# Optimization experiments

Hardware: AMD Instinct MI355X
Metric: run time of the kernel (lower is better)

The kernel has to match this reference:

```python
import jax, jax.numpy as jnp
import numpy as np
import math

B, S, E, H, FF = 8, 1024, 1024, 16, 4096
HD = E // H
N_DOM = 1024          # boolean-domain size used in the custom scale
LN_EPS = 1e-5


def _layernorm(x, g, b, eps=LN_EPS):
    mu = jnp.mean(x, axis=-1, keepdims=True)
    var = jnp.var(x, axis=-1, keepdims=True)
    return (x - mu) * jax.lax.rsqrt(var + eps) * g + b


def setup_inputs() -> dict:
    key = jax.random.key(0)
    ks = jax.random.split(key, 8)
    s_e = 1.0 / math.sqrt(E)
    s_f = 1.0 / math.sqrt(FF)
    return {
        "x": jax.random.normal(ks[0], (B, S, E), jnp.float32),
        "in_proj_w": jax.random.normal(ks[1], (3 * E, E), jnp.float32) * s_e,
        "out_proj_w": jax.random.normal(ks[2], (E, E), jnp.float32) * s_e,
        "ln1_g": jnp.ones((E,), jnp.float32),
        "ln1_b": jnp.zeros((E,), jnp.float32),
        "ln2_g": jnp.ones((E,), jnp.float32),
        "ln2_b": jnp.zeros((E,), jnp.float32),
        "w1": jax.random.normal(ks[3], (FF, E), jnp.float32) * s_e,
        "b1": jax.random.normal(ks[4], (FF,), jnp.float32) * 0.01,
        "w2": jax.random.normal(ks[5], (E, FF), jnp.float32) * s_f,
        "b2": jax.random.normal(ks[6], (E,), jnp.float32) * 0.01,
    }


def reference(x, in_proj_w, out_proj_w, ln1_g, ln1_b, ln2_g, ln2_b, w1, b1, w2, b2):
    # --- custom multi-head attention (bias=False, dropout=0) ---
    qkv = jnp.einsum("bse,fe->bsf", x, in_proj_w)              # [B,S,3E]
    q, k, v = jnp.split(qkv, 3, axis=-1)
    q = q.reshape(B, S, H, HD)
    k = k.reshape(B, S, H, HD)
    v = v.reshape(B, S, H, HD)
    # nonstandard scale: sqrt(1/head_dim) * 2 * log(N)
    scale = math.sqrt(1.0 / HD) * 2.0 * math.log(N_DOM)
    scores = jnp.einsum("bqhd,bkhd->bhqk", q * scale, k)       # [B,H,S,S]
    attn = jax.nn.softmax(scores, axis=-1)
    ctx = jnp.einsum("bhqk,bkhd->bqhd", attn, v).reshape(B, S, E)
    attn_out = jnp.einsum("bse,fe->bsf", ctx, out_proj_w)      # [B,S,E]
    # --- residual + norm + FFN + residual + norm ---
    h = _layernorm(x + attn_out, ln1_g, ln1_b)
    ff = jnp.einsum("bsf,ef->bse", jax.nn.relu(jnp.einsum("bse,fe->bsf", h, w1) + b1), w2) + b2
    return _layernorm(h + ff, ln2_g, ln2_b)
```

## Files before the change

kernel.cpp:

```cpp
#include <hip/hip_runtime.h>
#include <cstdint>
#include <cmath>


typedef _Float16 f16;
typedef _Float16 f16x8 __attribute__((ext_vector_type(8)));
typedef _Float16 f16x4 __attribute__((ext_vector_type(4)));
typedef __bf16   bf16;
typedef __bf16   bf16x8 __attribute__((ext_vector_type(8)));
typedef __bf16   bf16x4 __attribute__((ext_vector_type(4)));
typedef __bf16   bf16x2 __attribute__((ext_vector_type(2)));
typedef float    f32x4  __attribute__((ext_vector_type(4)));
typedef float    f32x16 __attribute__((ext_vector_type(16)));
typedef unsigned int uint2v __attribute__((ext_vector_type(2)));
typedef unsigned int u32x4v __attribute__((ext_vector_type(4)));

#define B_SZ  8
#define S_SZ  1024
#define E_SZ  1024
#define H_SZ  16
#define HD_SZ 64
#define FF_SZ 4096
#define MTOK  (B_SZ * S_SZ)

__device__ __forceinline__ void async_ld16(const void* g, void* l) {
  __builtin_amdgcn_global_load_lds(
      (const __attribute__((address_space(1))) void*)(uintptr_t)g,
      (__attribute__((address_space(3))) void*)(uint32_t)(uintptr_t)l,
      16, 0, 0);
}

template <int N>
__device__ __forceinline__ void wait_vm() {
  if constexpr (N == 0)      asm volatile("s_waitcnt vmcnt(0)" ::: "memory");
  else if constexpr (N == 3) asm volatile("s_waitcnt vmcnt(3)" ::: "memory");
  else if constexpr (N == 4) asm volatile("s_waitcnt vmcnt(4)" ::: "memory");
  else static_assert(N == 0 || N == 3 || N == 4, "unsupported vmcnt");
  __builtin_amdgcn_sched_barrier(0);
}

__device__ __forceinline__ void wait_lgkm0_fenced() {
  asm volatile("s_waitcnt lgkmcnt(0)" ::: "memory");
  __builtin_amdgcn_sched_barrier(0);
}

__device__ __forceinline__ void permswap(uint32_t& a, uint32_t& b) {
  uint2v r = __builtin_amdgcn_permlane32_swap(a, b, false, false);
  a = r[0];
  b = r[1];
}

__global__ void cast_all_kernel(const float* __restrict__ wqkv, const float* __restrict__ wo,
                                const float* __restrict__ w1, const float* __restrict__ w2,
                                const float* __restrict__ x,
                                f16* __restrict__ w_inb, f16* __restrict__ w_outb,
                                f16* __restrict__ w1b, f16* __restrict__ w2b,
                                f16* __restrict__ xb) {
  const int i = blockIdx.x * blockDim.x + threadIdx.x;
  const float* src;
  f16* dst;
  int off;
  if (i < 786432)       { src = wqkv; dst = w_inb;  off = i; }
  else if (i < 1048576) { src = wo;   dst = w_outb; off = i - 786432; }
  else if (i < 2097152) { src = w1;   dst = w1b;    off = i - 1048576; }
  else if (i < 3145728) { src = w2;   dst = w2b;    off = i - 2097152; }
  else                  { src = x;    dst = xb;     off = i - 3145728; }
  float4 f = ((const float4*)src)[off];
  f16x4 o = {(f16)f.x, (f16)f.y, (f16)f.z, (f16)f.w};
  ((f16x4*)dst)[off] = o;
}

template <int BN, bool OUT_F16, bool RELU>
__global__ __launch_bounds__(512, 2)
void gemm256(const f16* __restrict__ A, const f16* __restrict__ Bm,
             const float* __restrict__ bias, void* __restrict__ Cp,
             int M, int N, int K, int bf16_from_col) {
  static_assert(BN == 256 || BN == 128, "BN must be 256 or 128");
  static_assert(!(OUT_F16 && BN == 128), "f16 LDS epilogue requires BN==256");
  constexpr int NBCH  = (BN == 256) ? 2 : 1;
  constexpr int CHUNK = 4096;
  constexpr int NIF   = 2 + NBCH;
  constexpr int WN    = (BN == 256) ? 4 : 2;
  constexpr int FM    = (BN == 256) ? 8 : 4;

  __shared__ f16 lds[(8 + 4 * NBCH) * CHUNK];
  f16* Ab = lds;
  f16* Bb = lds + 8 * CHUNK;

  const int tid  = threadIdx.x;
  const int wave = tid >> 6;
  const int lane = tid & 63;
  const int quad = lane >> 4;
  const int l16  = lane & 15;

  const int wm  = wave / WN;
  const int wn  = wave % WN;
  const int ah  = (BN == 256) ? wm : (wm >> 1);
  const int amB = (BN == 256) ? 0 : (wm & 1) * 64;
  const int bh  = (BN == 256) ? (wn >> 1) : 0;
  const int bnB = (BN == 256) ? (wn & 1) * 64 : wn * 64;

  const int gx = N / BN;
  int bm, bn;
  {
    const int b   = blockIdx.x;
    const int nwg = gridDim.x;
    const int gm  = nwg / gx;
    if (((nwg & 63) == 0) && ((gx & 1) == 0) && ((gm & 3) == 0)) {
      const int xcd = b & 7;
      const int seq = b >> 3;
      const int st  = xcd + ((seq >> 3) << 3);
      const int pos = seq & 7;
      const int nstx = gx >> 1;
      bn = (st % nstx) * 2 + (pos & 1);
      bm = (st / nstx) * 4 + (pos >> 1);
    } else {
      int logical = b;
      if ((nwg & 7) == 0) logical = (logical & 7) * (nwg >> 3) + (logical >> 3);
      bn = logical % gx;
      bm = logical / gx;
    }
  }

  f32x4 acc[FM][4];
#pragma unroll
  for (int mi = 0; mi < FM; mi++)
#pragma unroll
    for (int ni = 0; ni < 4; ni++) acc[mi][ni] = (f32x4){0.f, 0.f, 0.f, 0.f};

  const int rr_s = tid >> 2;
  const int lo_s = (tid & 3) ^ ((rr_s >> 1) & 3);
  const int wofs = wave * 512;
  const f16* gAb = A  + ((size_t)bm * 256 + rr_s) * (size_t)K + lo_s * 8;
  const f16* gBb = Bm + ((size_t)bn * BN  + rr_s) * (size_t)K + lo_s * 8;

  auto stA = [&](int bb, int s, int h, int kt) {
    async_ld16(gAb + (size_t)h * 128 * K + kt * 64 + s * 32,
               Ab + ((((bb << 1) + s) << 1) + h) * CHUNK + wofs);
  };
  auto stB = [&](int bb, int s, int h, int kt) {
    async_ld16(gBb + (size_t)h * 128 * K + kt * 64 + s * 32,
               Bb + (((bb << 1) + s) * NBCH + h) * CHUNK + wofs);
  };
  auto rdFrag = [&](const f16* ch, int rr) -> f16x8 {
    return *(const f16x8*)&ch[rr * 32 + ((quad ^ ((rr >> 1) & 3)) << 3)];
  };

  const int NT = K >> 6;

#pragma unroll
  for (int s = 0; s < 2; s++) {
    stA(0, s, 0, 0);
    stA(0, s, 1, 0);
    stB(0, s, 0, 0);
    if constexpr (NBCH == 2) stB(0, s, 1, 0);
  }
  wait_vm<NIF>();
  __builtin_amdgcn_s_barrier();

  for (int t = 0; t < NT; t++) {
    const int cur = t & 1, oth = cur ^ 1;
    const bool last = (t == NT - 1);
#pragma unroll
    for (int s = 0; s < 2; s++) {
      const f16* Ach = Ab + ((((cur << 1) + s) << 1) + ah) * CHUNK;
      const f16* Bch = Bb + (((cur << 1) + s) * NBCH + bh) * CHUNK;

      f16x8 bfr[4], af[4];
#pragma unroll
      for (int ni = 0; ni < 4; ni++) bfr[ni] = rdFrag(Bch, bnB + ni * 16 + l16);
#pragma unroll
      for (int i = 0; i < 4; i++) af[i] = rdFrag(Ach, amB + i * 16 + l16);
      if (!last) {
        stA(oth, s, 0, t + 1);
        stA(oth, s, 1, t + 1);
        if constexpr (NBCH == 1) stB(oth, s, 0, t + 1);
      }
      __builtin_amdgcn_sched_barrier(0);
      __builtin_amdgcn_s_barrier();
      wait_lgkm0_fenced();
      __builtin_amdgcn_s_setprio(1);
#pragma unroll
      for (int i = 0; i < 4; i++)
#pragma unroll
        for (int ni = 0; ni < 4; ni++)
          acc[i][ni] = __builtin_amdgcn_mfma_f32_16x16x32_f16(bfr[ni], af[i], acc[i][ni], 0, 0, 0);
      __builtin_amdgcn_s_setprio(0);

      if constexpr (BN == 256) {
        __builtin_amdgcn_s_barrier();
#pragma unroll
        for (int i = 0; i < 4; i++) af[i] = rdFrag(Ach, amB + (4 + i) * 16 + l16);
        if (!last) {
          stB(oth, s, 0, t + 1);
          stB(oth, s, 1, t + 1);
        }
        __builtin_amdgcn_sched_barrier(0);
        __builtin_amdgcn_s_barrier();
        wait_lgkm0_fenced();
        __builtin_amdgcn_s_setprio(1);
#pragma unroll
        for (int i = 0; i < 4; i++)
#pragma unroll
          for (int ni = 0; ni < 4; ni++)
            acc[4 + i][ni] = __builtin_amdgcn_mfma_f32_16x16x32_f16(bfr[ni], af[i], acc[4 + i][ni], 0, 0, 0);
        __builtin_amdgcn_s_setprio(0);
      }

      if (!last) {
        wait_vm<NIF>();
        __builtin_amdgcn_s_barrier();
      } else if (s == 0) {
        wait_vm<0>();
        __builtin_amdgcn_s_barrier();
      }
    }
  }

  if constexpr (!OUT_F16) {
    const int rowG0 = bm * 256 + ((BN == 256) ? wm * 128 : wm * 64);
    const int colG0 = bn * BN + wn * 64;
    float* Cf = (float*)Cp;
#pragma unroll
    for (int ni = 0; ni < 4; ni++) {
      const int col = colG0 + ni * 16 + quad * 4;
      float4 bv = {0.f, 0.f, 0.f, 0.f};
      if (bias != nullptr) bv = *(const float4*)&bias[col];
#pragma unroll
      for (int mi = 0; mi < FM; mi++) {
        const int row = rowG0 + mi * 16 + l16;
        float v0 = acc[mi][ni][0] + bv.x;
        float v1 = acc[mi][ni][1] + bv.y;
        float v2 = acc[mi][ni][2] + bv.z;
        float v3 = acc[mi][ni][3] + bv.w;
        if (RELU) {
          v0 = fmaxf(v0, 0.f); v1 = fmaxf(v1, 0.f);
          v2 = fmaxf(v2, 0.f); v3 = fmaxf(v3, 0.f);
        }
        f32x4 o = {v0, v1, v2, v3};
        *(f32x4*)&Cf[(size_t)row * N + col] = o;
      }
    }
  } else {
    __syncthreads();
    {
      char* cb = (char*)lds;
      const int rowL0 = wm * 128;
      const int colL0 = wn * 64;
      const bool store_bf16 = (bn * BN >= bf16_from_col);
#pragma unroll
      for (int mi = 0; mi < FM; mi++) {
        const int row = rowL0 + mi * 16 + l16;
        const int sw  = row & 7;
#pragma unroll
        for (int ni = 0; ni < 4; ni++) {
          const int col = colL0 + ni * 16 + quad * 4;
          float4 bv = {0.f, 0.f, 0.f, 0.f};
          if (bias != nullptr) bv = *(const float4*)&bias[bn * BN + col];
          float v0 = acc[mi][ni][0] + bv.x;
          float v1 = acc[mi][ni][1] + bv.y;
          float v2 = acc[mi][ni][2] + bv.z;
          float v3 = acc[mi][ni][3] + bv.w;
          if (RELU) {
            v0 = fmaxf(v0, 0.f); v1 = fmaxf(v1, 0.f);
            v2 = fmaxf(v2, 0.f); v3 = fmaxf(v3, 0.f);
          }
          const int ch = (col >> 3) ^ sw;
          char* p = cb + row * 512 + (ch << 4) + ((quad & 1) << 3);
          if (store_bf16) {
            bf16x4 o = {(bf16)v0, (bf16)v1, (bf16)v2, (bf16)v3};
            *(bf16x4*)p = o;
          } else {
            f16x4 o = {(f16)v0, (f16)v1, (f16)v2, (f16)v3};
            *(f16x4*)p = o;
          }
        }
      }
    }
    __syncthreads();
    {
      const char* cb = (const char*)lds;
      const int rr0 = tid >> 5;
      const int cc  = tid & 31;
      const size_t rowBytes = (size_t)N * 2;
      char* gbase = (char*)Cp + (size_t)(bm * 256) * rowBytes
                  + (size_t)bn * BN * 2 + (size_t)cc * 16;
#pragma unroll
      for (int it = 0; it < 16; it++) {
        const int row = it * 16 + rr0;
        const int ch  = cc ^ (row & 7);
        u32x4v v = *(const u32x4v*)(cb + row * 512 + (ch << 4));
        *(u32x4v*)(gbase + (size_t)row * rowBytes) = v;
      }
    }
  }
  (void)M;
}

__global__ __launch_bounds__(256, 4)
void attn_kernel(const f16* __restrict__ qkv, f16* __restrict__ ctx,
                 float scale2, float c2) {
  __shared__ __align__(16) char pool[33280];
  f16*  Ks = (f16*)pool;
  bf16* Vt = (bf16*)(pool + 16384);

  const int tid  = threadIdx.x;
  const int wave = tid >> 6;
  const int lane = tid & 63;
  const int l31  = lane & 31;
  const int hi   = lane >> 5;

  const int flat = blockIdx.x;
  const int bh   = flat & 127;
  const int qt   = flat >> 7;
  const int b    = bh >> 4;
  const int h    = bh & 15;

  const int rs = 3 * E_SZ;
  const size_t tokbase = (size_t)b * S_SZ;

  const int su  = lane >> 3;
  const int soc = (lane & 7) ^ su;

  {
    const f16* gq = qkv + (tokbase + qt * 128 + wave * 8 + su) * (size_t)rs + h * HD_SZ + soc * 8;
#pragma unroll
    for (int i = 0; i < 4; i++)
      async_ld16(gq + (size_t)i * 32 * rs, pool + (i * 32 + wave * 8) * 128);
  }
  __syncthreads();

  f16x8 aq[4];
  {
    const int qrow = wave * 32 + l31;
    const f16 sc = (f16)scale2;
    const f16x8 sc8 = {sc, sc, sc, sc, sc, sc, sc, sc};
#pragma unroll
    for (int ks = 0; ks < 4; ks++) {
      f16x8 q = *(const f16x8*)&Ks[qrow * 64 + (((ks * 2 + hi) ^ (qrow & 7)) << 3)];
      aq[ks] = q * sc8;
    }
  }

  f16x8  kreg[4];
  bf16x8 vr0, vr1, vr2, vr3;
  const int vc  = (tid & 7) * 8;
  const int vk0 = (tid >> 3) * 4;
  {
    const f16* gk = qkv + (tokbase + wave * 8 + su) * (size_t)rs + E_SZ + h * HD_SZ + soc * 8;
#pragma unroll
    for (int i = 0; i < 4; i++) kreg[i] = *(const f16x8*)(gk + (size_t)i * 32 * rs);
    const bf16* gv = (const bf16*)qkv + (tokbase + vk0) * (size_t)rs + 2 * E_SZ + h * HD_SZ + vc;
    vr0 = *(const bf16x8*)(gv);
    vr1 = *(const bf16x8*)(gv + rs);
    vr2 = *(const bf16x8*)(gv + 2 * rs);
    vr3 = *(const bf16x8*)(gv + 3 * rs);
  }

  float Lp = 0.f;
  f32x16 oacc[2];
#pragma unroll
  for (int nb = 0; nb < 2; nb++)
#pragma unroll
    for (int i = 0; i < 16; i++) oacc[nb][i] = 0.f;

  const float negc2 = -c2;

  for (int t = 0; t < S_SZ / 128; t++) {
    __syncthreads();
    {
      const int kwr = (wave * 8 + su) * 64 + (lane & 7) * 8;
#pragma unroll
      for (int i = 0; i < 4; i++)
        *(f16x8*)&Ks[kwr + i * 32 * 64] = kreg[i];
    }
    {
#pragma unroll
      for (int e = 0; e < 8; e++) {
        bf16x4 pk = {vr0[e], vr1[e], vr2[e], vr3[e]};
        *(bf16x4*)&Vt[(vc + e) * 132 + vk0] = pk;
      }
    }
    __syncthreads();

    if (t < S_SZ / 128 - 1) {
      const f16* gk = qkv + (tokbase + (t + 1) * 128 + wave * 8 + su) * (size_t)rs + E_SZ + h * HD_SZ + soc * 8;
#pragma unroll
      for (int i = 0; i < 4; i++) kreg[i] = *(const f16x8*)(gk + (size_t)i * 32 * rs);
      const bf16* gv = (const bf16*)qkv + (tokbase + (t + 1) * 128 + vk0) * (size_t)rs + 2 * E_SZ + h * HD_SZ + vc;
      vr0 = *(const bf16x8*)(gv);
      vr1 = *(const bf16x8*)(gv + rs);
      vr2 = *(const bf16x8*)(gv + 2 * rs);
      vr3 = *(const bf16x8*)(gv + 3 * rs);
    }

#pragma unroll
    for (int nt = 0; nt < 4; nt++) {
      f32x16 sacc;
#pragma unroll
      for (int i = 0; i < 16; i++) sacc[i] = negc2;

      const int krow = nt * 32 + l31;
      __builtin_amdgcn_s_setprio(1);
#pragma unroll
      for (int ks = 0; ks < 4; ks++) {
        f16x8 kf = *(const f16x8*)&Ks[krow * 64 + (((ks * 2 + hi) ^ (krow & 7)) << 3)];
        sacc = __builtin_amdgcn_mfma_f32_32x32x16_f16(kf, aq[ks], sacc, 0, 0, 0);
      }
      __builtin_amdgcn_s_setprio(0);

      uint32_t w[8];
#pragma unroll
      for (int j = 0; j < 8; j++) {
        float p0 = exp2f(sacc[2 * j]);
        float p1 = exp2f(sacc[2 * j + 1]);
        Lp += p0 + p1;
        bf16x2 pk2 = {(bf16)p0, (bf16)p1};
        w[j] = __builtin_bit_cast(uint32_t, pk2);
      }
      permswap(w[0], w[2]);
      permswap(w[1], w[3]);
      permswap(w[4], w[6]);
      permswap(w[5], w[7]);
      u32x4v pe = {w[0], w[1], w[2], w[3]};
      u32x4v po = {w[4], w[5], w[6], w[7]};
      bf16x8 pa[2] = {__builtin_bit_cast(bf16x8, pe), __builtin_bit_cast(bf16x8, po)};

      __builtin_amdgcn_s_setprio(1);
#pragma unroll
      for (int nb = 0; nb < 2; nb++) {
        const int d = nb * 32 + l31;
#pragma unroll
        for (int kst = 0; kst < 2; kst++) {
          const int key = (nt * 2 + kst) * 16 + hi * 8;
          bf16x4 blo = *(const bf16x4*)&Vt[d * 132 + key];
          bf16x4 bhi = *(const bf16x4*)&Vt[d * 132 + key + 4];
          bf16x8 bv = __builtin_shufflevector(blo, bhi, 0, 1, 2, 3, 4, 5, 6, 7);
          oacc[nb] = __builtin_amdgcn_mfma_f32_32x32x16_bf16(pa[kst], bv, oacc[nb], 0, 0, 0);
        }
      }
      __builtin_amdgcn_s_setprio(0);
    }
  }

  float Lfull = Lp + __shfl_xor(Lp, 32, 64);
  const float inv = 1.f / Lfull;
#pragma unroll
  for (int r = 0; r < 16; r++) {
    const int qrow = (r & 3) + 8 * (r >> 2) + 4 * hi;
    const float invr = __shfl(inv, qrow, 32);
    const size_t row = tokbase + (size_t)qt * 128 + wave * 32 + qrow;
#pragma unroll
    for (int nb = 0; nb < 2; nb++)
      ctx[row * (size_t)E_SZ + h * HD_SZ + nb * 32 + l31] = (f16)(oacc[nb][r] * invr);
  }
}

__global__ void ln_kernel(const float* __restrict__ a, const float* __restrict__ res,
                          const float* __restrict__ g, const float* __restrict__ bta,
                          float* __restrict__ out32, f16* __restrict__ out16) {
  const int row  = blockIdx.x;
  const int tid  = threadIdx.x;
  const int wave = tid >> 6;
  const int lane = tid & 63;
  const size_t base = (size_t)row * 1024;
  const int c = tid * 4;

  float4 va = *(const float4*)&a[base + c];
  float4 vr = *(const float4*)&res[base + c];
  float v0 = va.x + vr.x, v1 = va.y + vr.y, v2 = va.z + vr.z, v3 = va.w + vr.w;

  __shared__ float r1[4], r2[4];
  float s = v0 + v1 + v2 + v3;
#pragma unroll
  for (int off = 32; off; off >>= 1) s += __shfl_xor(s, off, 64);
  if (lane == 0) r1[wave] = s;
  __syncthreads();
  const float mu = (r1[0] + r1[1] + r1[2] + r1[3]) * (1.f / 1024.f);

  float d0 = v0 - mu, d1 = v1 - mu, d2 = v2 - mu, d3 = v3 - mu;
  float ss = d0 * d0 + d1 * d1 + d2 * d2 + d3 * d3;
#pragma unroll
  for (int off = 32; off; off >>= 1) ss += __shfl_xor(ss, off, 64);
  if (lane == 0) r2[wave] = ss;
  __syncthreads();
  const float var = (r2[0] + r2[1] + r2[2] + r2[3]) * (1.f / 1024.f);
  const float rsq = rsqrtf(var + 1e-5f);

  float4 gg = *(const float4*)&g[c];
  float4 bb = *(const float4*)&bta[c];
  float o0 = d0 * rsq * gg.x + bb.x;
  float o1 = d1 * rsq * gg.y + bb.y;
  float o2 = d2 * rsq * gg.z + bb.z;
  float o3 = d3 * rsq * gg.w + bb.w;
  float4 o = {o0, o1, o2, o3};
  *(float4*)&out32[base + c] = o;
  if (out16 != nullptr) {
    f16x4 ob = {(f16)o0, (f16)o1, (f16)o2, (f16)o3};
    *(f16x4*)&out16[base + c] = ob;
  }
}

extern "C" void kernel_launch(void* const* d_in, const int* in_sizes, int n_in,
                              void* d_out, int out_size, void* d_ws, size_t ws_size,
                              hipStream_t stream) {
  const float* x    = (const float*)d_in[0];
  const float* wqkv = (const float*)d_in[1];
  const float* wo   = (const float*)d_in[2];
  const float* ln1g = (const float*)d_in[3];
  const float* ln1b = (const float*)d_in[4];
  const float* ln2g = (const float*)d_in[5];
  const float* ln2b = (const float*)d_in[6];
  const float* w1   = (const float*)d_in[7];
  const float* b1   = (const float*)d_in[8];
  const float* w2   = (const float*)d_in[9];
  const float* b2   = (const float*)d_in[10];
  float* out = (float*)d_out;

  char* ws = (char*)d_ws;
  f16* w_inb  = (f16*)(ws + 0);
  f16* w_outb = (f16*)(ws + 6291456);
  f16* w1b    = (f16*)(ws + 8388608);
  f16* w2b    = (f16*)(ws + 16777216);
  f16* xb     = (f16*)(ws + 25165824);
  f16* qkv    = (f16*)(ws + 41943040);
  f16* ctx    = (f16*)(ws + 92274688);
  f16* ff1    = (f16*)(ws + 41943040);
  float* tmp  = (float*)(ws + 109051904);
  float* hbuf = (float*)(ws + 142606336);
  f16* hb     = xb;

  const int NOBF = 1 << 30;

  cast_all_kernel<<<20480, 256, 0, stream>>>(wqkv, wo, w1, w2, x,
                                             w_inb, w_outb, w1b, w2b, xb);

  gemm256<256, true, false><<<(3 * E_SZ / 256) * (MTOK / 256), 512, 0, stream>>>(
      xb, w_inb, nullptr, qkv, MTOK, 3 * E_SZ, E_SZ, 2048);

  attn_kernel<<<1024, 256, 0, stream>>>(qkv, ctx, 2.5f, 60.0f);

  gemm256<128, false, false><<<(E_SZ / 128) * (MTOK / 256), 512, 0, stream>>>(
      ctx, w_outb, nullptr, tmp, MTOK, E_SZ, E_SZ, NOBF);

  ln_kernel<<<MTOK, 256, 0, stream>>>(tmp, x, ln1g, ln1b, hbuf, hb);

  gemm256<256, true, true><<<(FF_SZ / 256) * (MTOK / 256), 512, 0, stream>>>(
      hb, w1b, b1, ff1, MTOK, FF_SZ, E_SZ, NOBF);

  gemm256<128, false, false><<<(E_SZ / 128) * (MTOK / 256), 512, 0, stream>>>(
      ff1, w2b, b2, tmp, MTOK, E_SZ, FF_SZ, NOBF);

  ln_kernel<<<MTOK, 256, 0, stream>>>(tmp, hbuf, ln2g, ln2b, out, nullptr);

  (void)in_sizes; (void)n_in; (void)out_size; (void)ws_size;
}
```

Baseline: 484.2 us.

## Issue full next K-tile prefetch at iteration start and relax waits

Moves all async global-to-LDS loads for the next K tile to the top of each iteration, instead of spreading them between the MFMA phases. Waits on vmcnt are adjusted to per-half counts (2*NIF after the first half, NIF after the second), and one barrier in the BN=256 path is removed. The aim is to give loads more time in flight and cut synchronization. The cost is more outstanding loads at once, and the dropped barrier may affect LDS hazard safety.

Measured after the change: 513.9 us. 6.1% more time.

```diff
diff --git a/kernel.cpp b/kernel.cpp
--- a/kernel.cpp
+++ b/kernel.cpp
@@ -35,7 +35,10 @@
   if constexpr (N == 0)      asm volatile("s_waitcnt vmcnt(0)" ::: "memory");
   else if constexpr (N == 3) asm volatile("s_waitcnt vmcnt(3)" ::: "memory");
   else if constexpr (N == 4) asm volatile("s_waitcnt vmcnt(4)" ::: "memory");
-  else static_assert(N == 0 || N == 3 || N == 4, "unsupported vmcnt");
+  else if constexpr (N == 6) asm volatile("s_waitcnt vmcnt(6)" ::: "memory");
+  else if constexpr (N == 8) asm volatile("s_waitcnt vmcnt(8)" ::: "memory");
+  else static_assert(N == 0 || N == 3 || N == 4 || N == 6 || N == 8,
+                     "unsupported vmcnt");
   __builtin_amdgcn_sched_barrier(0);
 }
 
@@ -145,22 +148,28 @@
   auto rdFrag = [&](const f16* ch, int rr) -> f16x8 {
     return *(const f16x8*)&ch[rr * 32 + ((quad ^ ((rr >> 1) & 3)) << 3)];
   };
+  auto stageTile = [&](int bb, int kt) {
+#pragma unroll
+    for (int s = 0; s < 2; s++) {
+      stA(bb, s, 0, kt);
+      stA(bb, s, 1, kt);
+      stB(bb, s, 0, kt);
+      if constexpr (NBCH == 2) stB(bb, s, 1, kt);
+    }
+  };
 
   const int NT = K >> 6;
 
-#pragma unroll
-  for (int s = 0; s < 2; s++) {
-    stA(0, s, 0, 0);
-    stA(0, s, 1, 0);
-    stB(0, s, 0, 0);
-    if constexpr (NBCH == 2) stB(0, s, 1, 0);
-  }
+  stageTile(0, 0);
   wait_vm<NIF>();
   __builtin_amdgcn_s_barrier();
 
   for (int t = 0; t < NT; t++) {
     const int cur = t & 1, oth = cur ^ 1;
     const bool last = (t == NT - 1);
+
+    if (!last) stageTile(oth, t + 1);
+
 #pragma unroll
     for (int s = 0; s < 2; s++) {
       const f16* Ach = Ab + ((((cur << 1) + s) << 1) + ah) * CHUNK;
@@ -171,11 +180,6 @@
       for (int ni = 0; ni < 4; ni++) bfr[ni] = rdFrag(Bch, bnB + ni * 16 + l16);
 #pragma unroll
       for (int i = 0; i < 4; i++) af[i] = rdFrag(Ach, amB + i * 16 + l16);
-      if (!last) {
-        stA(oth, s, 0, t + 1);
-        stA(oth, s, 1, t + 1);
-        if constexpr (NBCH == 1) stB(oth, s, 0, t + 1);
-      }
       __builtin_amdgcn_sched_barrier(0);
       __builtin_amdgcn_s_barrier();
       wait_lgkm0_fenced();
@@ -191,12 +195,7 @@
         __builtin_amdgcn_s_barrier();
 #pragma unroll
         for (int i = 0; i < 4; i++) af[i] = rdFrag(Ach, amB + (4 + i) * 16 + l16);
-        if (!last) {
-          stB(oth, s, 0, t + 1);
-          stB(oth, s, 1, t + 1);
-        }
         __builtin_amdgcn_sched_barrier(0);
-        __builtin_amdgcn_s_barrier();
         wait_lgkm0_fenced();
         __builtin_amdgcn_s_setprio(1);
 #pragma unroll
@@ -207,11 +206,12 @@
         __builtin_amdgcn_s_setprio(0);
       }
 
-      if (!last) {
+      if (s == 0) {
+        if (!last) wait_vm<2 * NIF>();
+        else       wait_vm<0>();
+        __builtin_amdgcn_s_barrier();
+      } else if (!last) {
         wait_vm<NIF>();
-        __builtin_amdgcn_s_barrier();
-      } else if (s == 0) {
-        wait_vm<0>();
         __builtin_amdgcn_s_barrier();
       }
     }
```
